# Kernel optimization log

Measured on AMD Instinct MI355X. Metric: run time of the kernel, lower is better.

Reference implementation:

```python
import jax, jax.numpy as jnp
import numpy as np

B, S, D = 2, 2048, 1024
H, HD = 16, 64          # num_heads, head_dim = D // H
C = 8                   # subspace_dim of the equivariant relative-position basis
EPS = 1e-6              # flax LayerNorm default epsilon


def setup_inputs() -> dict:
    key = jax.random.key(0)
    ks = jax.random.split(key, 12)
    sd = 0.02
    return {
        "x": jax.random.normal(ks[0], (B, S, D), jnp.float32),
        "Q_basis": jax.random.normal(ks[1], (S, S, C), jnp.float32),
        "Wq": jax.random.normal(ks[2], (D, H, HD), jnp.float32) * sd,
        "bq": jnp.zeros((H, HD), jnp.float32),
        "Wk": jax.random.normal(ks[3], (D, H, HD), jnp.float32) * sd,
        "bk": jnp.zeros((H, HD), jnp.float32),
        "Wv": jax.random.normal(ks[4], (D, H, HD), jnp.float32) * sd,
        "bv": jnp.zeros((H, HD), jnp.float32),
        "q_ln_scale": jnp.ones((HD,), jnp.float32),
        "k_ln_scale": jnp.ones((HD,), jnp.float32),
        "relative_attn": jax.random.normal(ks[5], (C, H), jnp.float32) * sd,
        "Wo": jax.random.normal(ks[6], (H, HD, D), jnp.float32) * sd,
        "bo": jnp.zeros((D,), jnp.float32),
    }


def _layernorm(x, scale):
    # LayerNorm over last axis, use_bias=False
    mu = jnp.mean(x, axis=-1, keepdims=True)
    var = jnp.mean(jnp.square(x - mu), axis=-1, keepdims=True)
    return (x - mu) * jax.lax.rsqrt(var + EPS) * scale


def reference(x, Q_basis, Wq, bq, Wk, bk, Wv, bv,
              q_ln_scale, k_ln_scale, relative_attn, Wo, bo):
    # QKV projections: [B,S,D] x [D,H,HD] -> [B,S,H,HD]
    q = jnp.einsum('bsd,dhk->bshk', x, Wq) + bq
    k = jnp.einsum('bsd,dhk->bshk', x, Wk) + bk
    v = jnp.einsum('bsd,dhk->bshk', x, Wv) + bv
    # QK layernorm over head_dim
    q = _layernorm(q, q_ln_scale)
    k = _layernorm(k, k_ln_scale)
    # Learned relative-position bias: [C,H] x [S,S,C] -> [H,S,S]
    bias = jnp.einsum('ch,qkc->hqk', relative_attn, Q_basis)
    # Scaled dot-product attention with bias (matches nn.dot_product_attention)
    scores = jnp.einsum('bqhd,bkhd->bhqk', q, k) / jnp.sqrt(jnp.float32(HD))
    attn = jax.nn.softmax(scores + bias, axis=-1)
    ctx = jnp.einsum('bhqk,bkhd->bqhd', attn, v)
    # Output projection over (heads, head_dim) -> D
    return jnp.einsum('bqhd,hdo->bqo', ctx, Wo) + bo
```

## Files before the change

kernel.cpp:

```cpp
#include <hip/hip_runtime.h>

typedef float f32x4 __attribute__((ext_vector_type(4)));
typedef __bf16 bf16x8 __attribute__((ext_vector_type(8)));
typedef unsigned short u16x8 __attribute__((ext_vector_type(8)));
typedef unsigned short u16x4 __attribute__((ext_vector_type(4)));

#define AS1 __attribute__((address_space(1)))
#define AS3 __attribute__((address_space(3)))

static __device__ __forceinline__ void gll16(const void* g, void* l) {
  __builtin_amdgcn_global_load_lds((const AS1 void*)g, (AS3 void*)l, 16, 0, 0);
}

static __device__ __forceinline__ float bf2f(unsigned short u) {
  unsigned int x = ((unsigned int)u) << 16;
  float f; __builtin_memcpy(&f, &x, 4); return f;
}
static __device__ __forceinline__ unsigned short f2bf(float f) {
  __bf16 h = (__bf16)f;
  unsigned short u; __builtin_memcpy(&u, &h, 2); return u;
}

#define LOG2E 1.4426950408889634f
#define QSCALE (0.125f * LOG2E)

__global__ __launch_bounds__(256) void k_cvt_x(const float* __restrict__ x,
                                               unsigned short* __restrict__ xb) {
  int i = (blockIdx.x * 256 + threadIdx.x) * 4;
  float4 v = *(const float4*)(x + i);
  u16x4 o; o.x = f2bf(v.x); o.y = f2bf(v.y); o.z = f2bf(v.z); o.w = f2bf(v.w);
  *(u16x4*)(xb + i) = o;
}

__global__ __launch_bounds__(256) void k_transpose(const float* __restrict__ w0,
                                                   const float* __restrict__ w1,
                                                   const float* __restrict__ w2,
                                                   const float* __restrict__ w3,
                                                   unsigned short* __restrict__ dqkv,
                                                   unsigned short* __restrict__ dwo) {
  __shared__ float tile[32][33];
  int z = blockIdx.z;
  const float* src = (z == 0) ? w0 : (z == 1) ? w1 : (z == 2) ? w2 : w3;
  unsigned short* dst = (z < 3) ? (dqkv + (size_t)z * 1024 * 1024) : dwo;
  int tx = threadIdx.x, ty = threadIdx.y;
  int x0 = blockIdx.x * 32, y0 = blockIdx.y * 32;
#pragma unroll
  for (int i = 0; i < 4; ++i)
    tile[ty + 8 * i][tx] = src[(size_t)(y0 + ty + 8 * i) * 1024 + x0 + tx];
  __syncthreads();
#pragma unroll
  for (int i = 0; i < 4; ++i)
    dst[(size_t)(x0 + ty + 8 * i) * 1024 + y0 + tx] = f2bf(tile[tx][ty + 8 * i]);
}

__global__ __launch_bounds__(256) void k_bias(const float* __restrict__ Qb,
                                              const float* __restrict__ R,
                                              unsigned short* __restrict__ bias) {
  __shared__ float Rs[8][16];
  int t = threadIdx.x;
  if (t < 128) Rs[t >> 4][t & 15] = R[t] * LOG2E;
  __syncthreads();
  int q = blockIdx.x;
  int k = t * 8;
  const float* src = Qb + ((size_t)q * 2048 + k) * 8;
  float a[8][8];
#pragma unroll
  for (int kk = 0; kk < 8; ++kk) {
    float4 lo = *(const float4*)(src + kk * 8);
    float4 hi = *(const float4*)(src + kk * 8 + 4);
    a[kk][0] = lo.x; a[kk][1] = lo.y; a[kk][2] = lo.z; a[kk][3] = lo.w;
    a[kk][4] = hi.x; a[kk][5] = hi.y; a[kk][6] = hi.z; a[kk][7] = hi.w;
  }
#pragma unroll
  for (int h = 0; h < 16; ++h) {
    u16x8 o;
#pragma unroll
    for (int kk = 0; kk < 8; ++kk) {
      float s = 0.f;
#pragma unroll
      for (int c = 0; c < 8; ++c) s += a[kk][c] * Rs[c][h];
      o[kk] = f2bf(s);
    }
    *(u16x8*)(bias + ((size_t)h * 2048 + q) * 2048 + k) = o;
  }
}

__global__ __launch_bounds__(256) void k_qkv(const unsigned short* __restrict__ xb,
                                             const unsigned short* __restrict__ wt,
                                             const float* __restrict__ bq,
                                             const float* __restrict__ bk,
                                             const float* __restrict__ bv,
                                             const float* __restrict__ qls,
                                             const float* __restrict__ kls,
                                             unsigned short* __restrict__ qo,
                                             unsigned short* __restrict__ kqo,
                                             unsigned short* __restrict__ vo) {
  __shared__ __align__(16) unsigned short As[8192];
  __shared__ __align__(16) unsigned short Bs[8192];
  const int tid = threadIdx.x;
  const int w = tid >> 6, lane = tid & 63, quad = lane >> 4, lx = lane & 15;
  const int m0 = blockIdx.y * 128, n0 = blockIdx.x * 128;
  const int wrow = w >> 1, wcol = w & 1;

  f32x4 acc[4][4];
#pragma unroll
  for (int i = 0; i < 4; ++i)
#pragma unroll
    for (int j = 0; j < 4; ++j) acc[i][j] = (f32x4){0.f, 0.f, 0.f, 0.f};

  const unsigned short* ga = xb + (size_t)(m0 + 32 * w + (lane >> 2)) * 1024 + (lane & 3) * 8;
  const unsigned short* gb = wt + (size_t)(n0 + 32 * w + (lane >> 2)) * 1024 + (lane & 3) * 8;

  gll16(ga, As + w * 1024);
  gll16(ga + 16 * 1024, As + w * 1024 + 512);
  gll16(gb, Bs + w * 1024);
  gll16(gb + 16 * 1024, Bs + w * 1024 + 512);
  __syncthreads();

  for (int kt = 0; kt < 32; ++kt) {
    const int cur = kt & 1;
    if (kt < 31) {
      const int kofs = (kt + 1) * 32;
      unsigned short* lan = As + (cur ^ 1) * 4096 + w * 1024;
      unsigned short* lbn = Bs + (cur ^ 1) * 4096 + w * 1024;
      gll16(ga + kofs, lan);
      gll16(ga + kofs + 16 * 1024, lan + 512);
      gll16(gb + kofs, lbn);
      gll16(gb + kofs + 16 * 1024, lbn + 512);
    }
    const unsigned short* ac = As + cur * 4096;
    const unsigned short* bc = Bs + cur * 4096;
    bf16x8 af[4], bfr[4];
#pragma unroll
    for (int i = 0; i < 4; ++i)
      af[i] = *(const bf16x8*)&ac[(64 * wrow + 16 * i + lx) * 32 + quad * 8];
#pragma unroll
    for (int j = 0; j < 4; ++j)
      bfr[j] = *(const bf16x8*)&bc[(64 * wcol + 16 * j + lx) * 32 + quad * 8];
    __builtin_amdgcn_s_setprio(1);
#pragma unroll
    for (int i = 0; i < 4; ++i)
#pragma unroll
      for (int j = 0; j < 4; ++j)
        acc[i][j] = __builtin_amdgcn_mfma_f32_16x16x32_bf16(af[i], bfr[j], acc[i][j], 0, 0, 0);
    __builtin_amdgcn_s_setprio(0);
    __syncthreads();
  }

  const int colbase = n0 + 64 * wcol;
  const int region = colbase >> 10;
  const int h = (colbase & 1023) >> 6;
  const float* pbp = (region == 0) ? bq : (region == 1) ? bk : bv;
  float pb[4];
#pragma unroll
  for (int j = 0; j < 4; ++j) pb[j] = pbp[h * 64 + j * 16 + lx];

  if (region == 2) {
#pragma unroll
    for (int i = 0; i < 4; ++i) {
#pragma unroll
      for (int rr = 0; rr < 4; ++rr) {
        int m = m0 + 64 * wrow + 16 * i + quad * 4 + rr;
        int b = m >> 11, s = m & 2047;
        unsigned short* dst = vo + ((size_t)b * 16 + h) * 64 * 2048 + s;
#pragma unroll
        for (int j = 0; j < 4; ++j)
          dst[(size_t)(j * 16 + lx) * 2048] = f2bf(acc[i][j][rr] + pb[j]);
      }
    }
  } else {
    const float fac = region ? 1.0f : QSCALE;
    float scl[4];
    const float* lsp = region ? kls : qls;
#pragma unroll
    for (int j = 0; j < 4; ++j) scl[j] = lsp[j * 16 + lx] * fac;
    unsigned short* base = region ? kqo : qo;
#pragma unroll
    for (int i = 0; i < 4; ++i) {
#pragma unroll
      for (int rr = 0; rr < 4; ++rr) {
        int m = m0 + 64 * wrow + 16 * i + quad * 4 + rr;
        int b = m >> 11, s = m & 2047;
        float v0 = acc[i][0][rr] + pb[0];
        float v1 = acc[i][1][rr] + pb[1];
        float v2 = acc[i][2][rr] + pb[2];
        float v3 = acc[i][3][rr] + pb[3];
        float s1 = v0 + v1 + v2 + v3;
        float s2 = v0 * v0 + v1 * v1 + v2 * v2 + v3 * v3;
#pragma unroll
        for (int d = 1; d < 16; d <<= 1) {
          s1 += __shfl_xor(s1, d, 64);
          s2 += __shfl_xor(s2, d, 64);
        }
        float mu = s1 * 0.015625f;
        float var = s2 * 0.015625f - mu * mu;
        float ri = __builtin_amdgcn_rsqf(var + 1e-6f);
        unsigned short* dst = base + (((size_t)b * 16 + h) * 2048 + s) * 64;
        dst[0 * 16 + lx] = f2bf((v0 - mu) * ri * scl[0]);
        dst[1 * 16 + lx] = f2bf((v1 - mu) * ri * scl[1]);
        dst[2 * 16 + lx] = f2bf((v2 - mu) * ri * scl[2]);
        dst[3 * 16 + lx] = f2bf((v3 - mu) * ri * scl[3]);
      }
    }
  }
}

__global__ __launch_bounds__(256) void k_attn(const unsigned short* __restrict__ qp,
                                              const unsigned short* __restrict__ kp,
                                              const unsigned short* __restrict__ vp,
                                              const unsigned short* __restrict__ bp,
                                              unsigned short* __restrict__ ctx) {
  __shared__ __align__(16) unsigned short QPs[4096];
  __shared__ __align__(16) unsigned short Ks[8192];
  __shared__ __align__(16) unsigned short Vs[8192];
  const int tid = threadIdx.x;
  const int w = tid >> 6, lane = tid & 63, quad = lane >> 4, lx = lane & 15;
  const int lx7 = lane & 7;
  const int qt = blockIdx.x, h = blockIdx.y, b = blockIdx.z;
  const int q0 = qt * 64;
  const size_t bh = (size_t)b * 16 + h;

  const unsigned short* qg = qp + (bh * 2048 + q0) * 64;
  gll16(qg + w * 512 + lane * 8, QPs + w * 512);
  gll16(qg + 2048 + w * 512 + lane * 8, QPs + 2048 + w * 512);

  const unsigned short* kg = kp + bh * 2048 * 64;
  const unsigned short* vg = vp + bh * 64 * 2048;
  const unsigned short* bg = bp + ((size_t)h * 2048 + q0 + 16 * w + quad * 4) * 2048 + lx;

  const int rA = 16 * w + (lane >> 3);
  const int cA = (lane & 7) ^ (rA & 7);
  const unsigned short* kgA = kg + (size_t)rA * 64 + cA * 8;
  const unsigned short* kgB = kg + (size_t)(rA + 8) * 64 + cA * 8;
  const unsigned short* vgA = vg + (size_t)rA * 2048 + cA * 8;
  const unsigned short* vgB = vg + (size_t)(rA + 8) * 2048 + cA * 8;

  gll16(kgA, Ks + w * 1024);
  gll16(kgB, Ks + w * 1024 + 512);
  gll16(vgA, Vs + w * 1024);
  gll16(vgB, Vs + w * 1024 + 512);
  unsigned short bu[4][4], bun[4][4];
#pragma unroll
  for (int rr = 0; rr < 4; ++rr)
#pragma unroll
    for (int j = 0; j < 4; ++j) bu[rr][j] = bg[(size_t)rr * 2048 + j * 16];

  __syncthreads();

  bf16x8 qf[2];
#pragma unroll
  for (int hh = 0; hh < 2; ++hh)
    qf[hh] = *(const bf16x8*)&QPs[(16 * w + lx) * 64 + hh * 32 + quad * 8];

  float l_run[4] = {0.f, 0.f, 0.f, 0.f};
  f32x4 acco[4];
#pragma unroll
  for (int j = 0; j < 4; ++j) acco[j] = (f32x4){0.f, 0.f, 0.f, 0.f};

  for (int kt = 0; kt < 32; ++kt) {
    const int cur = kt & 1;
    const unsigned short* kc = Ks + cur * 4096;
    const unsigned short* vc = Vs + cur * 4096;
    if (kt < 31) {
      const size_t k1 = (size_t)(kt + 1) * 64;
      unsigned short* kn = Ks + (cur ^ 1) * 4096 + w * 1024;
      unsigned short* vn = Vs + (cur ^ 1) * 4096 + w * 1024;
      gll16(kgA + k1 * 64, kn);
      gll16(kgB + k1 * 64, kn + 512);
      gll16(vgA + k1, vn);
      gll16(vgB + k1, vn + 512);
#pragma unroll
      for (int rr = 0; rr < 4; ++rr)
#pragma unroll
        for (int j = 0; j < 4; ++j) bun[rr][j] = bg[(size_t)rr * 2048 + k1 + j * 16];
    }

    f32x4 accs[4];
#pragma unroll
    for (int j = 0; j < 4; ++j)
#pragma unroll
      for (int rr = 0; rr < 4; ++rr) accs[j][rr] = bf2f(bu[rr][j]);
    __builtin_amdgcn_s_setprio(1);
#pragma unroll
    for (int j = 0; j < 4; ++j) {
#pragma unroll
      for (int hh = 0; hh < 2; ++hh) {
        bf16x8 kf = *(const bf16x8*)&kc[(j * 16 + lx) * 64 + ((hh * 4 + quad) ^ lx7) * 8];
        accs[j] = __builtin_amdgcn_mfma_f32_16x16x32_bf16(qf[hh], kf, accs[j], 0, 0, 0);
      }
    }
    __builtin_amdgcn_s_setprio(0);

#pragma unroll
    for (int rr = 0; rr < 4; ++rr) {
      float p0 = __builtin_amdgcn_exp2f(accs[0][rr]);
      float p1 = __builtin_amdgcn_exp2f(accs[1][rr]);
      float p2 = __builtin_amdgcn_exp2f(accs[2][rr]);
      float p3 = __builtin_amdgcn_exp2f(accs[3][rr]);
      l_run[rr] += (p0 + p1) + (p2 + p3);
      const int q = quad * 4 + rr;
      const int swz = q & 7;
      const int ch = lx >> 3;
      unsigned short* pw = QPs + w * 1024 + q * 64 + (lx & 7);
      pw[((ch ^ swz) << 3)]       = f2bf(p0);
      pw[(((ch + 2) ^ swz) << 3)] = f2bf(p1);
      pw[(((ch + 4) ^ swz) << 3)] = f2bf(p2);
      pw[(((ch + 6) ^ swz) << 3)] = f2bf(p3);
    }
    __asm__ volatile("s_waitcnt lgkmcnt(0)" ::: "memory");
    bf16x8 pf[2];
#pragma unroll
    for (int kh = 0; kh < 2; ++kh)
      pf[kh] = *(const bf16x8*)&QPs[w * 1024 + lx * 64 + (((kh * 4 + quad) ^ (lx & 7)) << 3)];
    __builtin_amdgcn_s_setprio(1);
#pragma unroll
    for (int j = 0; j < 4; ++j) {
#pragma unroll
      for (int kh = 0; kh < 2; ++kh) {
        bf16x8 vf = *(const bf16x8*)&vc[(j * 16 + lx) * 64 + ((kh * 4 + quad) ^ lx7) * 8];
        acco[j] = __builtin_amdgcn_mfma_f32_16x16x32_bf16(pf[kh], vf, acco[j], 0, 0, 0);
      }
    }
    __builtin_amdgcn_s_setprio(0);
    __syncthreads();
#pragma unroll
    for (int rr = 0; rr < 4; ++rr)
#pragma unroll
      for (int j = 0; j < 4; ++j) bu[rr][j] = bun[rr][j];
  }

#pragma unroll
  for (int rr = 0; rr < 4; ++rr) {
    float l = l_run[rr];
#pragma unroll
    for (int d = 1; d < 16; d <<= 1) l += __shfl_xor(l, d, 64);
    float rl = __builtin_amdgcn_rcpf(l);
    int s = q0 + 16 * w + quad * 4 + rr;
    unsigned short* dst = ctx + (((size_t)b * 2048 + s) * 16 + h) * 64;
#pragma unroll
    for (int j = 0; j < 4; ++j) dst[j * 16 + lx] = f2bf(acco[j][rr] * rl);
  }
}

__global__ __launch_bounds__(256) void k_out(const unsigned short* __restrict__ cx,
                                             const unsigned short* __restrict__ wt,
                                             const float* __restrict__ bo,
                                             float* __restrict__ out) {
  __shared__ __align__(16) unsigned short As[8192];
  __shared__ __align__(16) unsigned short Bs[4096];
  const int tid = threadIdx.x;
  const int w = tid >> 6, lane = tid & 63, quad = lane >> 4, lx = lane & 15;
  const int m0 = blockIdx.y * 128, n0 = blockIdx.x * 64;
  const int wrow = w >> 1, wcol = w & 1;

  f32x4 acc[4][2];
#pragma unroll
  for (int i = 0; i < 4; ++i)
#pragma unroll
    for (int j = 0; j < 2; ++j) acc[i][j] = (f32x4){0.f, 0.f, 0.f, 0.f};

  const unsigned short* ga = cx + (size_t)(m0 + 32 * w + (lane >> 2)) * 1024 + (lane & 3) * 8;
  const unsigned short* gb = wt + (size_t)(n0 + 16 * w + (lane >> 2)) * 1024 + (lane & 3) * 8;

  gll16(ga, As + w * 1024);
  gll16(ga + 16 * 1024, As + w * 1024 + 512);
  gll16(gb, Bs + w * 512);
  __syncthreads();

  for (int kt = 0; kt < 32; ++kt) {
    const int cur = kt & 1;
    if (kt < 31) {
      const int kofs = (kt + 1) * 32;
      unsigned short* lan = As + (cur ^ 1) * 4096 + w * 1024;
      gll16(ga + kofs, lan);
      gll16(ga + kofs + 16 * 1024, lan + 512);
      gll16(gb + kofs, Bs + (cur ^ 1) * 2048 + w * 512);
    }
    const unsigned short* ac = As + cur * 4096;
    const unsigned short* bc = Bs + cur * 2048;
    bf16x8 af[4], bfr[2];
#pragma unroll
    for (int i = 0; i < 4; ++i)
      af[i] = *(const bf16x8*)&ac[(64 * wrow + 16 * i + lx) * 32 + quad * 8];
#pragma unroll
    for (int j = 0; j < 2; ++j)
      bfr[j] = *(const bf16x8*)&bc[(32 * wcol + 16 * j + lx) * 32 + quad * 8];
    __builtin_amdgcn_s_setprio(1);
#pragma unroll
    for (int i = 0; i < 4; ++i)
#pragma unroll
      for (int j = 0; j < 2; ++j)
        acc[i][j] = __builtin_amdgcn_mfma_f32_16x16x32_bf16(af[i], bfr[j], acc[i][j], 0, 0, 0);
    __builtin_amdgcn_s_setprio(0);
    __syncthreads();
  }

  const int colbase = n0 + 32 * wcol;
  float bb[2];
#pragma unroll
  for (int j = 0; j < 2; ++j) bb[j] = bo[colbase + j * 16 + lx];
#pragma unroll
  for (int i = 0; i < 4; ++i) {
#pragma unroll
    for (int rr = 0; rr < 4; ++rr) {
      int m = m0 + 64 * wrow + 16 * i + quad * 4 + rr;
      float* dst = out + (size_t)m * 1024 + colbase;
#pragma unroll
      for (int j = 0; j < 2; ++j) dst[j * 16 + lx] = acc[i][j][rr] + bb[j];
    }
  }
}

extern "C" void kernel_launch(void* const* d_in, const int* in_sizes, int n_in,
                              void* d_out, int out_size, void* d_ws, size_t ws_size,
                              hipStream_t stream) {
  (void)in_sizes; (void)n_in; (void)out_size; (void)ws_size;
  const float* x   = (const float*)d_in[0];
  const float* Qb  = (const float*)d_in[1];
  const float* Wq  = (const float*)d_in[2];
  const float* bq  = (const float*)d_in[3];
  const float* Wk  = (const float*)d_in[4];
  const float* bk  = (const float*)d_in[5];
  const float* Wv  = (const float*)d_in[6];
  const float* bv  = (const float*)d_in[7];
  const float* qls = (const float*)d_in[8];
  const float* kls = (const float*)d_in[9];
  const float* Ra  = (const float*)d_in[10];
  const float* Wo  = (const float*)d_in[11];
  const float* bo  = (const float*)d_in[12];
  float* out = (float*)d_out;

  char* ws = (char*)d_ws;
  unsigned short* xb    = (unsigned short*)(ws + 0);
  unsigned short* wqkvt = (unsigned short*)(ws + 8388608);
  unsigned short* wot   = (unsigned short*)(ws + 14680064);
  unsigned short* qb    = (unsigned short*)(ws + 16777216);
  unsigned short* kb    = (unsigned short*)(ws + 25165824);
  unsigned short* vtb   = (unsigned short*)(ws + 33554432);
  unsigned short* ctxb  = (unsigned short*)(ws + 41943040);
  unsigned short* biasb = (unsigned short*)(ws + 50331648);

  k_cvt_x<<<4096, 256, 0, stream>>>(x, xb);
  k_transpose<<<dim3(32, 32, 4), dim3(32, 8), 0, stream>>>(Wq, Wk, Wv, Wo, wqkvt, wot);
  k_bias<<<2048, 256, 0, stream>>>(Qb, Ra, biasb);
  k_qkv<<<dim3(24, 32), 256, 0, stream>>>(xb, wqkvt, bq, bk, bv, qls, kls, qb, kb, vtb);
  k_attn<<<dim3(32, 16, 2), 256, 0, stream>>>(qb, kb, vtb, biasb, ctxb);
  k_out<<<dim3(16, 32), 256, 0, stream>>>(ctxb, wot, bo, out);
}
```

Before: 435.1 us.

## Store bias in MFMA-fragment-tiled layout for vectorized attention loads

The bias kernel now writes the bf16 relative-position bias in a layout tiled to match the MFMA accumulator fragment order of the attention kernel, so each lane holds its 16 bias values contiguously. The attention kernel then loads them with two 16-byte vector loads per tile instead of 16 scattered 2-byte loads. The bias kernel's reads of Q_basis become less contiguous per thread, which may cost some efficiency there.

```diff
diff --git a/kernel.cpp b/kernel.cpp
--- a/kernel.cpp
+++ b/kernel.cpp
@@ -60,28 +60,37 @@
   int t = threadIdx.x;
   if (t < 128) Rs[t >> 4][t & 15] = R[t] * LOG2E;
   __syncthreads();
-  int q = blockIdx.x;
-  int k = t * 8;
-  const float* src = Qb + ((size_t)q * 2048 + k) * 8;
-  float a[8][8];
-#pragma unroll
-  for (int kk = 0; kk < 8; ++kk) {
-    float4 lo = *(const float4*)(src + kk * 8);
-    float4 hi = *(const float4*)(src + kk * 8 + 4);
-    a[kk][0] = lo.x; a[kk][1] = lo.y; a[kk][2] = lo.z; a[kk][3] = lo.w;
-    a[kk][4] = hi.x; a[kk][5] = hi.y; a[kk][6] = hi.z; a[kk][7] = hi.w;
-  }
-#pragma unroll
-  for (int h = 0; h < 16; ++h) {
-    u16x8 o;
-#pragma unroll
-    for (int kk = 0; kk < 8; ++kk) {
-      float s = 0.f;
-#pragma unroll
-      for (int c = 0; c < 8; ++c) s += a[kk][c] * Rs[c][h];
-      o[kk] = f2bf(s);
-    }
-    *(u16x8*)(bias + ((size_t)h * 2048 + q) * 2048 + k) = o;
+  const int lane = t & 63, hg = t >> 6;
+  const int quad = lane >> 4, lx = lane & 15;
+  const int kt = blockIdx.x;
+  const int qg = blockIdx.y;
+
+  u16x8 out[4][2];
+#pragma unroll
+  for (int j = 0; j < 4; ++j) {
+#pragma unroll
+    for (int rr = 0; rr < 4; ++rr) {
+      const int q = qg * 16 + quad * 4 + rr;
+      const int k = kt * 64 + j * 16 + lx;
+      const float* ap = Qb + ((size_t)q * 2048 + k) * 8;
+      float4 c0 = *(const float4*)ap;
+      float4 c1 = *(const float4*)(ap + 4);
+#pragma unroll
+      for (int hh = 0; hh < 4; ++hh) {
+        const int h = hg * 4 + hh;
+        float s = c0.x * Rs[0][h] + c0.y * Rs[1][h] + c0.z * Rs[2][h] + c0.w * Rs[3][h]
+                + c1.x * Rs[4][h] + c1.y * Rs[5][h] + c1.z * Rs[6][h] + c1.w * Rs[7][h];
+        const int v = j * 4 + rr;
+        out[hh][v >> 3][v & 7] = f2bf(s);
+      }
+    }
+  }
+#pragma unroll
+  for (int hh = 0; hh < 4; ++hh) {
+    const int h = hg * 4 + hh;
+    unsigned short* dst = bias + ((((size_t)h * 128 + qg) * 32 + kt) * 64 + lane) * 16;
+    *(u16x8*)dst = out[hh][0];
+    *(u16x8*)(dst + 8) = out[hh][1];
   }
 }
 
@@ -226,7 +235,7 @@
 
   const unsigned short* kg = kp + bh * 2048 * 64;
   const unsigned short* vg = vp + bh * 64 * 2048;
-  const unsigned short* bg = bp + ((size_t)h * 2048 + q0 + 16 * w + quad * 4) * 2048 + lx;
+  const unsigned short* bgt = bp + ((((size_t)h * 128 + (q0 >> 4) + w) * 32) * 64 + lane) * 16;
 
   const int rA = 16 * w + (lane >> 3);
   const int cA = (lane & 7) ^ (rA & 7);
@@ -239,11 +248,9 @@
   gll16(kgB, Ks + w * 1024 + 512);
   gll16(vgA, Vs + w * 1024);
   gll16(vgB, Vs + w * 1024 + 512);
-  unsigned short bu[4][4], bun[4][4];
-#pragma unroll
-  for (int rr = 0; rr < 4; ++rr)
-#pragma unroll
-    for (int j = 0; j < 4; ++j) bu[rr][j] = bg[(size_t)rr * 2048 + j * 16];
+  u16x8 bu_lo = *(const u16x8*)(bgt);
+  u16x8 bu_hi = *(const u16x8*)(bgt + 8);
+  u16x8 bun_lo = bu_lo, bun_hi = bu_hi;
 
   __syncthreads();
 
@@ -269,17 +276,16 @@
       gll16(kgB + k1 * 64, kn + 512);
       gll16(vgA + k1, vn);
       gll16(vgB + k1, vn + 512);
+      bun_lo = *(const u16x8*)(bgt + (size_t)(kt + 1) * 1024);
+      bun_hi = *(const u16x8*)(bgt + (size_t)(kt + 1) * 1024 + 8);
+    }
+
+    f32x4 accs[4];
+#pragma unroll
+    for (int j = 0; j < 4; ++j)
 #pragma unroll
       for (int rr = 0; rr < 4; ++rr)
-#pragma unroll
-        for (int j = 0; j < 4; ++j) bun[rr][j] = bg[(size_t)rr * 2048 + k1 + j * 16];
-    }
-
-    f32x4 accs[4];
-#pragma unroll
-    for (int j = 0; j < 4; ++j)
-#pragma unroll
-      for (int rr = 0; rr < 4; ++rr) accs[j][rr] = bf2f(bu[rr][j]);
+        accs[j][rr] = bf2f((j < 2) ? bu_lo[(j & 1) * 4 + rr] : bu_hi[(j & 1) * 4 + rr]);
     __builtin_amdgcn_s_setprio(1);
 #pragma unroll
     for (int j = 0; j < 4; ++j) {
@@ -323,10 +329,8 @@
     }
     __builtin_amdgcn_s_setprio(0);
     __syncthreads();
-#pragma unroll
-    for (int rr = 0; rr < 4; ++rr)
-#pragma unroll
-      for (int j = 0; j < 4; ++j) bu[rr][j] = bun[rr][j];
+    bu_lo = bun_lo;
+    bu_hi = bun_hi;
   }
 
 #pragma unroll
@@ -442,7 +446,7 @@
 
   k_cvt_x<<<4096, 256, 0, stream>>>(x, xb);
   k_transpose<<<dim3(32, 32, 4), dim3(32, 8), 0, stream>>>(Wq, Wk, Wv, Wo, wqkvt, wot);
-  k_bias<<<2048, 256, 0, stream>>>(Qb, Ra, biasb);
+  k_bias<<<dim3(32, 128), 256, 0, stream>>>(Qb, Ra, biasb);
   k_qkv<<<dim3(24, 32), 256, 0, stream>>>(xb, wqkvt, bq, bk, bv, qls, kls, qb, kb, vtb);
   k_attn<<<dim3(32, 16, 2), 256, 0, stream>>>(qb, kb, vtb, biasb, ctxb);
   k_out<<<dim3(16, 32), 256, 0, stream>>>(ctxb, wot, bo, out);
```

After: 414.7 us. 4.7% less time.
